# Performance work log

Measured on AMD Instinct MI355X. Metric: run time of the kernel, lower is better.

## Reference

```python
import jax, jax.numpy as jnp
import numpy as np

SLOPE = 10.0
NTR = 4.0
DTR = 0.0
DELTA = 3
MARG = 2


def _gt(x):
    return jax.nn.sigmoid(x * SLOPE)


def setup_inputs() -> dict:
    key = jax.random.key(0)
    x = jax.random.uniform(key, (16, 3, 512, 512), dtype=jnp.float32)
    return {"x": x}


def reference(x):
    B, C, H, W = x.shape
    d = DELTA
    # zero-pad H and W by delta (matches the two torch.cat calls)
    im_b = jnp.pad(x, ((0, 0), (0, 0), (d, d), (d, d)))

    roll_hw = lambda s: jnp.roll(im_b, s, axis=(2, 3))
    diff_11 = roll_hw((1, 1)) - im_b
    diff_nn11 = roll_hw((-1, -1)) - im_b
    diff_01 = roll_hw((0, 1)) - im_b
    diff_n01 = roll_hw((0, -1)) - im_b
    diff_10 = roll_hw((1, 0)) - im_b
    diff_n10 = roll_hw((-1, 0)) - im_b
    diff_n11 = roll_hw((-1, 1)) - im_b
    diff_1n1 = roll_hw((1, -1)) - im_b

    # NOTE: the original rolls the diff tensors over dims (1,2) = (channel, H).
    # We reproduce that exactly for faithfulness.
    rl = lambda t, s: jnp.roll(t, s, axis=(1, 2))

    ad_10 = jnp.abs(diff_10)
    ad_10 = ad_10 * _gt(ad_10 - DTR)
    e10a = _gt(ad_10 - jnp.abs(diff_01)) + _gt(ad_10 - jnp.abs(diff_n01)) + _gt(ad_10 - jnp.abs(diff_n10))
    # original repeats the roll(diff_01) term twice
    e10b = (_gt(ad_10 - jnp.abs(rl(diff_01, (1, 0))))
            + _gt(ad_10 - jnp.abs(rl(diff_n01, (1, 0))))
            + _gt(ad_10 - jnp.abs(rl(diff_01, (1, 0)))))
    g10 = _gt(e10a + e10b - NTR)
    e10 = g10 * _gt(diff_10)
    e10n = g10 * _gt(-diff_10)

    ad_01 = jnp.abs(diff_01)
    ad_01 = ad_01 * _gt(ad_10 - DTR)  # original uses ad_10 here (faithful)
    e01a = _gt(ad_01 - jnp.abs(diff_10)) + _gt(ad_01 - jnp.abs(diff_n10)) + _gt(ad_01 - jnp.abs(diff_n01))
    e01b = (_gt(ad_01 - jnp.abs(rl(diff_10, (0, 1))))
            + _gt(ad_01 - jnp.abs(rl(diff_n10, (0, 1))))
            + _gt(ad_01 - jnp.abs(rl(diff_01, (0, 1)))))
    g01 = _gt(e01a + e01b - NTR)
    e01 = g01 * _gt(diff_01)
    e01n = g01 * _gt(diff_01)  # original uses +diff_01 for both (faithful)

    ad_11 = jnp.abs(diff_11)
    ad_11 = ad_11 * _gt(ad_11 - DTR)
    e11a = _gt(ad_11 - jnp.abs(diff_n11)) + _gt(ad_11 - jnp.abs(diff_1n1)) + _gt(ad_11 - jnp.abs(diff_nn11))
    e11b = (_gt(ad_11 - jnp.abs(rl(diff_n11, (1, 1))))
            + _gt(ad_11 - jnp.abs(rl(diff_1n1, (1, 1))))
            + _gt(ad_11 - jnp.abs(rl(diff_11, (1, 1)))))
    g11 = _gt(e11a + e11b - NTR)
    e11 = g11 * _gt(diff_11)
    e11n = g11 * _gt(-diff_11)

    ad_n11 = jnp.abs(diff_n11)
    ad_n11 = ad_n11 * (ad_n11 > DTR).astype(x.dtype)  # hard threshold here (faithful)
    en11a = _gt(ad_n11 - jnp.abs(diff_11)) + _gt(ad_n11 - jnp.abs(diff_1n1)) + _gt(ad_n11 - jnp.abs(diff_nn11))
    en11b = (_gt(ad_n11 - jnp.abs(rl(diff_11, (-1, 1))))
             + _gt(ad_n11 - jnp.abs(rl(diff_n11, (-1, 1))))
             + _gt(ad_n11 - jnp.abs(rl(diff_n11, (-1, 1)))))
    gn11 = _gt(en11a + en11b - NTR)
    en11 = gn11 * _gt(diff_n11)
    en11n = gn11 * _gt(-diff_n11)

    def crop_pad(e):
        # interior crop back to HxW minus margins, zeros elsewhere
        c = e[:, :, d + MARG:d + H - MARG, d + MARG:d + W - MARG]
        return jnp.pad(c, ((0, 0), (0, 0), (MARG, MARG), (MARG, MARG)))

    edges = jnp.stack([crop_pad(e) for e in (e10, e10n, e01, e01n, e11, e11n, en11, en11n)], axis=2)
    # (B, C, 8, H, W) -> (B, 8*C, H, W) in torch's reshape order (C-major)
    return edges.reshape(B, C * 8, H, W)
```

## Files before the change

### kernel.cpp

```cpp
#include <hip/hip_runtime.h>

#define HH 512
#define WW 512
#define KSL 14.426950408889634f
#define FOURK 57.707801635558536f

typedef float f4 __attribute__((ext_vector_type(4)));

__device__ __forceinline__ float sig_arg(float arg) {
    float e = __builtin_amdgcn_exp2f(arg);
    return __builtin_amdgcn_rcpf(1.0f + e);
}
__device__ __forceinline__ float QE(float x) {
    return __builtin_amdgcn_exp2f(KSL * fabsf(x));
}
__device__ __forceinline__ float term(float qx, float p) {
    return __builtin_amdgcn_rcpf(fmaf(qx, p, 1.0f));
}

__global__ __launch_bounds__(256, 2) void edge_kernel(const float* __restrict__ x,
                                                      float* __restrict__ out) {
    const int tx = threadIdx.x & 63;
    const int ty = threadIdx.x >> 6;
    const int w0 = blockIdx.x * 256 + tx * 4;
    const int h  = blockIdx.y * 4 + ty;
    const int z  = blockIdx.z;
    const int b  = z / 3;
    const int c  = z - 3 * b;

    float* outp = out + (((size_t)(b * 24 + c * 8) * HH + h) * WW + w0);
    const int PL = HH * WW;

    if (h < 2 || h >= HH - 2) {
        const f4 zf = {0.f, 0.f, 0.f, 0.f};
        #pragma unroll
        for (int k = 0; k < 8; ++k)
            __builtin_nontemporal_store(zf, (f4*)(outp + k * PL));
        return;
    }

    const int cm = (c + 2) % 3, cp = (c + 1) % 3;
    const int wl = (w0 == 0) ? 0 : (w0 - 1);
    const int wr = (w0 + 4 >= WW) ? (WW - 1) : (w0 + 4);

    const float* bas = x + (size_t)b * 3 * HH * WW + (size_t)(h - 2) * WW;

    float S[4][6], M[3][6], P[3][6];
    {
        const float* rp = bas + (size_t)c * (HH * WW);
        #pragma unroll
        for (int r = 0; r < 4; ++r) {
            const float* row = rp + r * WW;
            const f4 m = *(const f4*)(row + w0);
            S[r][1] = m.x; S[r][2] = m.y; S[r][3] = m.z; S[r][4] = m.w;
            if (r > 0) { S[r][0] = row[wl]; S[r][5] = row[wr]; }
        }
    }
    {
        const float* rp = bas + (size_t)cm * (HH * WW);
        #pragma unroll
        for (int r = 0; r < 3; ++r) {
            const float* row = rp + r * WW;
            const f4 m = *(const f4*)(row + w0);
            M[r][1] = m.x; M[r][2] = m.y; M[r][3] = m.z; M[r][4] = m.w;
            if (r != 1) { M[r][0] = row[wl]; M[r][5] = row[wr]; }
        }
    }
    {
        const float* rp = bas + (size_t)cp * (HH * WW);
        #pragma unroll
        for (int r = 0; r < 3; ++r) {
            const float* row = rp + r * WW;
            const f4 m = *(const f4*)(row + w0);
            P[r][1] = m.x; P[r][2] = m.y; P[r][3] = m.z; P[r][4] = m.w;
            if (r != 1) { P[r][0] = row[wl]; }
        }
    }

    float acc[8][4];
    #pragma unroll
    for (int q = 0; q < 4; ++q) {
        const float v = S[2][q + 1], u = S[1][q + 1];
        const float d10   = u           - v;
        const float dn10  = S[3][q + 1] - v;
        const float d01   = S[2][q]     - v;
        const float dn01  = S[2][q + 2] - v;
        const float d11   = S[1][q]     - v;
        const float dnn11 = S[3][q + 2] - v;
        const float dn11  = S[3][q]     - v;
        const float d1n1  = S[1][q + 2] - v;
        const float r_d10 = S[0][q + 1] - u;
        const float r_d01 = S[1][q]     - u;

        const float A01m   = M[2][q]     - M[2][q + 1];
        const float An01m  = M[2][q + 2] - M[2][q + 1];
        const float rA11m  = M[0][q]     - M[1][q + 1];
        const float rAn11m = M[2][q]     - M[1][q + 1];
        const float rA1n1m = M[0][q + 2] - M[1][q + 1];
        const float rA11p  = P[0][q]     - P[1][q + 1];
        const float rAn11p = P[2][q]     - P[1][q + 1];

        const float q10    = QE(d10),    qn10   = QE(dn10);
        const float q01    = QE(d01),    qn01   = QE(dn01);
        const float q11    = QE(d11),    qdn11  = QE(dn11);
        const float q1n1   = QE(d1n1),   qnn11  = QE(dnn11);
        const float qr10   = QE(r_d10),  qr01   = QE(r_d01);
        const float qA01m  = QE(A01m),   qAn01m = QE(An01m);
        const float qA11m  = QE(rA11m),  qAn11m = QE(rAn11m);
        const float qA1n1m = QE(rA1n1m);
        const float qA11p  = QE(rA11p),  qAn11p = QE(rAn11p);

        const float msk = ((w0 + q) >= 2 && (w0 + q) < WW - 2) ? 1.0f : 0.0f;

        const float a10  = fabsf(d10);
        const float r10  = __builtin_amdgcn_rcpf(1.0f + q10);
        const float om10 = 1.0f - r10;
        const float ad10 = a10 * om10;
        const float P10  = __builtin_amdgcn_exp2f(-KSL * ad10);
        const float e10s = term(q01, P10) + term(qn01, P10) + term(qn10, P10)
                         + 2.0f * term(qA01m, P10)
                         + term(qAn01m, P10);
        const float g10 = msk * sig_arg(fmaf(e10s, -KSL, FOURK));
        const float s10 = (d10 >= 0.0f) ? om10 : r10;
        acc[0][q] = g10 * s10;
        acc[1][q] = fmaf(-s10, g10, g10);

        const float sad10 = __builtin_amdgcn_rcpf(1.0f + P10);
        const float ad01  = fabsf(d01) * sad10;
        const float P01   = __builtin_amdgcn_exp2f(-KSL * ad01);
        const float e01s = 2.0f * term(q10, P01)
                         + term(qn10, P01) + term(qn01, P01)
                         + term(qr10, P01) + term(qr01, P01);
        const float g01 = msk * sig_arg(fmaf(e01s, -KSL, FOURK));
        const float r01 = __builtin_amdgcn_rcpf(1.0f + q01);
        const float s01 = (d01 >= 0.0f) ? (1.0f - r01) : r01;
        const float e01 = g01 * s01;
        acc[2][q] = e01;
        acc[3][q] = e01;

        const float a11  = fabsf(d11);
        const float r11  = __builtin_amdgcn_rcpf(1.0f + q11);
        const float om11 = 1.0f - r11;
        const float ad11 = a11 * om11;
        const float P11  = __builtin_amdgcn_exp2f(-KSL * ad11);
        const float e11s = term(qdn11, P11) + term(q1n1, P11) + term(qnn11, P11)
                         + term(qAn11m, P11) + term(qA1n1m, P11) + term(qA11m, P11);
        const float g11 = msk * sig_arg(fmaf(e11s, -KSL, FOURK));
        const float s11 = (d11 >= 0.0f) ? om11 : r11;
        acc[4][q] = g11 * s11;
        acc[5][q] = fmaf(-s11, g11, g11);

        const float Pn11 = __builtin_amdgcn_exp2f(-KSL * fabsf(dn11));
        const float en11s = term(q11, Pn11) + term(q1n1, Pn11) + term(qnn11, Pn11)
                          + term(qA11p, Pn11)
                          + 2.0f * term(qAn11p, Pn11);
        const float gn11 = msk * sig_arg(fmaf(en11s, -KSL, FOURK));
        const float rn   = __builtin_amdgcn_rcpf(1.0f + qdn11);
        const float sn11 = (dn11 >= 0.0f) ? (1.0f - rn) : rn;
        acc[6][q] = gn11 * sn11;
        acc[7][q] = fmaf(-sn11, gn11, gn11);
    }

    #pragma unroll
    for (int k = 0; k < 8; ++k) {
        const f4 o = {acc[k][0], acc[k][1], acc[k][2], acc[k][3]};
        __builtin_nontemporal_store(o, (f4*)(outp + k * PL));
    }
}

extern "C" void kernel_launch(void* const* d_in, const int* in_sizes, int n_in,
                              void* d_out, int out_size, void* d_ws, size_t ws_size,
                              hipStream_t stream) {
    const float* x = (const float*)d_in[0];
    float* out = (float*)d_out;
    dim3 grid(WW / 256, HH / 4, 16 * 3);
    dim3 block(256);
    edge_kernel<<<grid, block, 0, stream>>>(x, out);
}
```

Before: 448.1 us.

## Process two pixels per thread with one full row per block and swizzled row order

Each thread now computes 2 output pixels instead of 4, and each 256-thread block covers a full 512-wide row. Blocks are mapped to rows through a bit swizzle that spreads neighbouring block indices across distant rows. Launch bounds rise to 4 blocks per CU to raise occupancy via fewer registers per thread. The cost is smaller vector accesses (float2), proportionally more halo loads per output, and less L2 row reuse between consecutive blocks.

```diff
diff --git a/kernel.cpp b/kernel.cpp
--- a/kernel.cpp
+++ b/kernel.cpp
@@ -5,7 +5,7 @@
 #define KSL 14.426950408889634f
 #define FOURK 57.707801635558536f
 
-typedef float f4 __attribute__((ext_vector_type(4)));
+typedef float f2 __attribute__((ext_vector_type(2)));
 
 __device__ __forceinline__ float sig_arg(float arg) {
     float e = __builtin_amdgcn_exp2f(arg);
@@ -18,13 +18,13 @@
     return __builtin_amdgcn_rcpf(fmaf(qx, p, 1.0f));
 }
 
-__global__ __launch_bounds__(256, 2) void edge_kernel(const float* __restrict__ x,
+__global__ __launch_bounds__(256, 4) void edge_kernel(const float* __restrict__ x,
                                                       float* __restrict__ out) {
-    const int tx = threadIdx.x & 63;
-    const int ty = threadIdx.x >> 6;
-    const int w0 = blockIdx.x * 256 + tx * 4;
-    const int h  = blockIdx.y * 4 + ty;
-    const int z  = blockIdx.z;
+    const int t  = threadIdx.x;
+    const int w0 = t * 2;
+    const int hs = blockIdx.x;
+    const int h  = ((hs & 7) << 6) | (hs >> 3);
+    const int z  = blockIdx.y;
     const int b  = z / 3;
     const int c  = z - 3 * b;
 
@@ -32,54 +32,52 @@
     const int PL = HH * WW;
 
     if (h < 2 || h >= HH - 2) {
-        const f4 zf = {0.f, 0.f, 0.f, 0.f};
+        const f2 zf = {0.f, 0.f};
         #pragma unroll
         for (int k = 0; k < 8; ++k)
-            __builtin_nontemporal_store(zf, (f4*)(outp + k * PL));
+            __builtin_nontemporal_store(zf, (f2*)(outp + k * PL));
         return;
     }
 
     const int cm = (c + 2) % 3, cp = (c + 1) % 3;
     const int wl = (w0 == 0) ? 0 : (w0 - 1);
-    const int wr = (w0 + 4 >= WW) ? (WW - 1) : (w0 + 4);
+    const int wr = (w0 + 2 >= WW) ? (WW - 1) : (w0 + 2);
 
-    const float* bas = x + (size_t)b * 3 * HH * WW + (size_t)(h - 2) * WW;
-
-    float S[4][6], M[3][6], P[3][6];
+    float S[4][4], M[3][4], P[3][4];
     {
-        const float* rp = bas + (size_t)c * (HH * WW);
+        const float* rp = x + (((size_t)(b * 3 + c) * HH + (h - 2)) * WW);
         #pragma unroll
         for (int r = 0; r < 4; ++r) {
             const float* row = rp + r * WW;
-            const f4 m = *(const f4*)(row + w0);
-            S[r][1] = m.x; S[r][2] = m.y; S[r][3] = m.z; S[r][4] = m.w;
-            if (r > 0) { S[r][0] = row[wl]; S[r][5] = row[wr]; }
+            const f2 m = *(const f2*)(row + w0);
+            S[r][1] = m.x; S[r][2] = m.y;
+            if (r > 0) { S[r][0] = row[wl]; S[r][3] = row[wr]; }
         }
     }
     {
-        const float* rp = bas + (size_t)cm * (HH * WW);
+        const float* rp = x + (((size_t)(b * 3 + cm) * HH + (h - 2)) * WW);
         #pragma unroll
         for (int r = 0; r < 3; ++r) {
             const float* row = rp + r * WW;
-            const f4 m = *(const f4*)(row + w0);
-            M[r][1] = m.x; M[r][2] = m.y; M[r][3] = m.z; M[r][4] = m.w;
-            if (r != 1) { M[r][0] = row[wl]; M[r][5] = row[wr]; }
+            const f2 m = *(const f2*)(row + w0);
+            M[r][1] = m.x; M[r][2] = m.y;
+            if (r != 1) { M[r][0] = row[wl]; M[r][3] = row[wr]; }
         }
     }
     {
-        const float* rp = bas + (size_t)cp * (HH * WW);
+        const float* rp = x + (((size_t)(b * 3 + cp) * HH + (h - 2)) * WW);
         #pragma unroll
         for (int r = 0; r < 3; ++r) {
             const float* row = rp + r * WW;
-            const f4 m = *(const f4*)(row + w0);
-            P[r][1] = m.x; P[r][2] = m.y; P[r][3] = m.z; P[r][4] = m.w;
+            const f2 m = *(const f2*)(row + w0);
+            P[r][1] = m.x; P[r][2] = m.y;
             if (r != 1) { P[r][0] = row[wl]; }
         }
     }
 
-    float acc[8][4];
+    float acc[8][2];
     #pragma unroll
-    for (int q = 0; q < 4; ++q) {
+    for (int q = 0; q < 2; ++q) {
         const float v = S[2][q + 1], u = S[1][q + 1];
         const float d10   = u           - v;
         const float dn10  = S[3][q + 1] - v;
@@ -163,8 +161,8 @@
 
     #pragma unroll
     for (int k = 0; k < 8; ++k) {
-        const f4 o = {acc[k][0], acc[k][1], acc[k][2], acc[k][3]};
-        __builtin_nontemporal_store(o, (f4*)(outp + k * PL));
+        const f2 o = {acc[k][0], acc[k][1]};
+        __builtin_nontemporal_store(o, (f2*)(outp + k * PL));
     }
 }
 
@@ -173,7 +171,7 @@
                               hipStream_t stream) {
     const float* x = (const float*)d_in[0];
     float* out = (float*)d_out;
-    dim3 grid(WW / 256, HH / 4, 16 * 3);
+    dim3 grid(HH, 16 * 3);
     dim3 block(256);
     edge_kernel<<<grid, block, 0, stream>>>(x, out);
 }
```

New measurement: 460.0 us. +2.7%, slower.
